# Kernel tuning notes

Hardware: AMD Instinct MI355X
Metric: run time of the kernel (lower is better)

The kernel has to match this reference:

```python
import jax, jax.numpy as jnp
import numpy as np

B, CIN, COUT, H, KS = 16, 64, 64, 224, 7


def setup_inputs() -> dict:
    key = jax.random.key(0)
    k1, k2 = jax.random.split(key)
    x = jax.random.normal(k1, (B, CIN, H, H), dtype=jnp.float32)
    # kaiming_uniform_ default (a=0, fan_in mode): bound = sqrt(6 / fan_in)
    fan_in = CIN * KS * KS
    bound = float(np.sqrt(6.0 / fan_in))
    kernel = jax.random.uniform(k2, (COUT, CIN, KS, KS), minval=-bound, maxval=bound, dtype=jnp.float32)
    return {"input": x, "kernel": kernel}


def _kernel_spectrum(k2d, n):
    # Pad kernel to the optical plane size (n x n), centered, then ifftshift so the
    # frequency-domain product implements a centered circular convolution (4f system).
    ks = k2d.shape[-1]
    s = (n - ks) // 2
    pad = jnp.zeros(k2d.shape[:-2] + (n, n), k2d.dtype)
    pad = pad.at[..., s:s + ks, s:s + ks].set(k2d)
    return jnp.fft.fft2(jnp.fft.ifftshift(pad, axes=(-2, -1)))


def reference(input, kernel):
    n = input.shape[-1]
    # Original loop bug: in_channel index is always 0, so
    # out[b,oc] = optConv2d(sum_ic input[b,ic], kernel[oc,0])
    kf = _kernel_spectrum(kernel[:, 0], n)          # [O, H, W] complex
    sf = jnp.fft.fft2(input.sum(axis=1))            # [B, H, W] complex
    out = jnp.fft.ifft2(sf[:, None] * kf[None]).real  # [B, O, H, W]
    return out.astype(input.dtype)
```

## Files before the change

### kernel.cpp

```cpp
#include <hip/hip_runtime.h>
#include <hip/hip_bf16.h>

#define Hn 224
#define HWn (224*224)
#define B_ 16
#define CIN_ 64
#define COUT_ 64
#define PR 230
#define PC 240
#define PHW (PR*PC)
#define GUARD 1024
#define WOFF (4*1024*1024)

typedef __attribute__((ext_vector_type(4)))  float f32x4;
typedef __attribute__((ext_vector_type(8)))  short bf16x8;
typedef __attribute__((ext_vector_type(16))) float f32x16;

__global__ __launch_bounds__(256) void chan_sum_kernel(const float* __restrict__ x,
                                                       float* __restrict__ Sp) {
    int idx = blockIdx.x * 256 + threadIdx.x;
    const int npix4 = B_ * HWn / 4;
    if (idx >= npix4) return;
    const int s4 = HWn / 4;
    int b  = idx / s4;
    int p4 = idx - b * s4;
    const f32x4* xb = (const f32x4*)x + (size_t)b * CIN_ * s4 + p4;

    f32x4 a0 = __builtin_nontemporal_load(xb + 0 * s4);
    f32x4 a1 = __builtin_nontemporal_load(xb + 1 * s4);
    f32x4 a2 = __builtin_nontemporal_load(xb + 2 * s4);
    f32x4 a3 = __builtin_nontemporal_load(xb + 3 * s4);
    #pragma unroll 4
    for (int c = 4; c < CIN_; c += 4) {
        a0 += __builtin_nontemporal_load(xb + (size_t)(c + 0) * s4);
        a1 += __builtin_nontemporal_load(xb + (size_t)(c + 1) * s4);
        a2 += __builtin_nontemporal_load(xb + (size_t)(c + 2) * s4);
        a3 += __builtin_nontemporal_load(xb + (size_t)(c + 3) * s4);
    }
    f32x4 r = (a0 + a1) + (a2 + a3);

    int y  = p4 / 56;
    int xq = p4 - y * 56;
    float* dst = Sp + (size_t)b * PHW + (size_t)(y + 2) * PC + 2 + xq * 4;
    dst[0] = r.x; dst[1] = r.y; dst[2] = r.z; dst[3] = r.w;
}

__global__ __launch_bounds__(256) void halo_kernel(float* __restrict__ Sp) {
    const int perB = 224 * 6 + 6 * 230;
    int i = blockIdx.x * 256 + threadIdx.x;
    if (i >= perB * B_) return;
    int b = i / perB, t = i - b * perB;
    float* S = Sp + (size_t)b * PHW;
    if (t < 1344) {
        int j = t / 6, c = t - 6 * j;
        int pr = j + 2;
        int p, sp;
        if (c < 2) { p = c;       sp = 224 + c; }
        else       { p = 224 + c; sp = c;       }
        S[pr * PC + p] = S[pr * PC + sp];
    } else {
        t -= 1344;
        int rr = t / 230, p = t - 230 * rr;
        int pr  = (rr < 2) ? rr       : 224 + rr;
        int spr = (rr < 2) ? 224 + rr : rr;
        int sp  = (p < 2) ? p + 224 : (p >= 226 ? p - 224 : p);
        S[pr * PC + p] = S[spr * PC + sp];
    }
}

__global__ __launch_bounds__(256) void wprep_kernel(const float* __restrict__ K,
                                                    unsigned short* __restrict__ W) {
    int i = blockIdx.x * 256 + threadIdx.x;
    if (i >= 64 * 64) return;
    int oc = i >> 6, kk = i & 63;
    int ky = kk >> 3, kx = kk & 7;
    float v = (ky < 7 && kx < 7) ? K[(size_t)oc * (CIN_ * 49) + ky * 7 + kx] : 0.0f;
    __hip_bfloat16 h = __float2bfloat16(v);
    W[i] = *(unsigned short*)&h;
}

__global__ __launch_bounds__(128, 4) void conv_mfma(const float* __restrict__ Sp,
                                                    const unsigned short* __restrict__ W,
                                                    float* __restrict__ out) {
    const int yg = blockIdx.x;
    const int b  = blockIdx.y;
    const int wv = threadIdx.x >> 6;
    const int l  = threadIdx.x & 63;
    const int y   = yg * 2 + wv;
    const int lo5 = l & 31;
    const int hi  = l >> 5;

    bf16x8 afrag[2][4];
    #pragma unroll
    for (int g = 0; g < 2; ++g)
        #pragma unroll
        for (int c = 0; c < 4; ++c)
            afrag[g][c] = *(const bf16x8*)(W + ((g * 32 + lo5) * 64 + c * 16 + hi * 8));

    const float* Sb = Sp + (size_t)b * PHW;
    float* outb = out + (size_t)b * COUT_ * HWn + (size_t)y * Hn;

    for (int xt = 0; xt < 7; ++xt) {
        const int x0 = xt * 32;

        f32x16 acc0, acc1;
        #pragma unroll
        for (int i = 0; i < 16; ++i) { acc0[i] = 0.0f; acc1[i] = 0.0f; }

        #pragma unroll
        for (int c = 0; c < 4; ++c) {
            const int rowg = y + 6 - (2 * c + hi);
            const float* rp = Sb + rowg * PC + x0 + 6 + lo5;
            union { int i[4]; bf16x8 v; } bu;
            #pragma unroll
            for (int j = 0; j < 4; ++j) {
                float flo = rp[-(2 * j)];
                float fhi = rp[-(2 * j) - 1];
                asm("v_cvt_pk_bf16_f32 %0, %1, %2" : "=v"(bu.i[j]) : "v"(flo), "v"(fhi));
            }
            acc0 = __builtin_amdgcn_mfma_f32_32x32x16_bf16(afrag[0][c], bu.v, acc0, 0, 0, 0);
            acc1 = __builtin_amdgcn_mfma_f32_32x32x16_bf16(afrag[1][c], bu.v, acc1, 0, 0, 0);
        }

        #pragma unroll
        for (int r = 0; r < 16; ++r) {
            const int row = (r & 3) + 8 * (r >> 2) + 4 * hi;
            outb[(size_t)row        * HWn + x0 + lo5] = acc0[r];
            outb[(size_t)(32 + row) * HWn + x0 + lo5] = acc1[r];
        }
    }
}

extern "C" void kernel_launch(void* const* d_in, const int* in_sizes, int n_in,
                              void* d_out, int out_size, void* d_ws, size_t ws_size,
                              hipStream_t stream) {
    const float* x = (const float*)d_in[0];
    const float* K = (const float*)d_in[1];
    float* out = (float*)d_out;
    float* Sp = (float*)d_ws + GUARD;
    unsigned short* W = (unsigned short*)((char*)d_ws + WOFF);

    const int npix4 = B_ * HWn / 4;
    chan_sum_kernel<<<(npix4 + 255) / 256, 256, 0, stream>>>(x, Sp);

    const int haloN = B_ * (224 * 6 + 6 * 230);
    halo_kernel<<<(haloN + 255) / 256, 256, 0, stream>>>(Sp);

    wprep_kernel<<<16, 256, 0, stream>>>(K, W);

    dim3 g2(112, 16);
    conv_mfma<<<g2, 128, 0, stream>>>(Sp, W, out);
}
```

Measured before the change: 83.90 us.

## Fuse halo fill into channel sum and weight prep into conv kernel

The circular-wrap halo of the padded sum plane is now written directly by the channel-sum threads that own the edge pixels, which removes the separate halo kernel. The bf16 weight fragments are built inside the conv kernel straight from the fp32 kernel tensor, which removes the weight-prep kernel and its workspace buffer. The intent is to cut two kernel launches and their serialization gaps. In exchange, edge threads in the sum kernel diverge, and every conv block repeats the strided loads and conversion of the weights.

```diff
diff --git a/kernel.cpp b/kernel.cpp
--- a/kernel.cpp
+++ b/kernel.cpp
@@ -10,7 +10,6 @@
 #define PC 240
 #define PHW (PR*PC)
 #define GUARD 1024
-#define WOFF (4*1024*1024)
 
 typedef __attribute__((ext_vector_type(4)))  float f32x4;
 typedef __attribute__((ext_vector_type(8)))  short bf16x8;
@@ -38,49 +37,51 @@
         a3 += __builtin_nontemporal_load(xb + (size_t)(c + 3) * s4);
     }
     f32x4 r = (a0 + a1) + (a2 + a3);
+    float v0 = r.x, v1 = r.y, v2 = r.z, v3 = r.w;
 
     int y  = p4 / 56;
-    int xq = p4 - y * 56;
-    float* dst = Sp + (size_t)b * PHW + (size_t)(y + 2) * PC + 2 + xq * 4;
-    dst[0] = r.x; dst[1] = r.y; dst[2] = r.z; dst[3] = r.w;
-}
+    int x0 = (p4 - y * 56) * 4;
+    float* Sb = Sp + (size_t)b * PHW;
 
-__global__ __launch_bounds__(256) void halo_kernel(float* __restrict__ Sp) {
-    const int perB = 224 * 6 + 6 * 230;
-    int i = blockIdx.x * 256 + threadIdx.x;
-    if (i >= perB * B_) return;
-    int b = i / perB, t = i - b * perB;
-    float* S = Sp + (size_t)b * PHW;
-    if (t < 1344) {
-        int j = t / 6, c = t - 6 * j;
-        int pr = j + 2;
-        int p, sp;
-        if (c < 2) { p = c;       sp = 224 + c; }
-        else       { p = 224 + c; sp = c;       }
-        S[pr * PC + p] = S[pr * PC + sp];
-    } else {
-        t -= 1344;
-        int rr = t / 230, p = t - 230 * rr;
-        int pr  = (rr < 2) ? rr       : 224 + rr;
-        int spr = (rr < 2) ? 224 + rr : rr;
-        int sp  = (p < 2) ? p + 224 : (p >= 226 ? p - 224 : p);
-        S[pr * PC + p] = S[spr * PC + sp];
+    float* dst = Sb + (size_t)(y + 2) * PC + 2 + x0;
+    dst[0] = v0; dst[1] = v1; dst[2] = v2; dst[3] = v3;
+
+    if (y < 4) {
+        float* d = Sb + (size_t)(y + 226) * PC + 2 + x0;
+        d[0] = v0; d[1] = v1; d[2] = v2; d[3] = v3;
+    }
+    if (y >= 222) {
+        float* d = Sb + (size_t)(y - 222) * PC + 2 + x0;
+        d[0] = v0; d[1] = v1; d[2] = v2; d[3] = v3;
+    }
+    if (x0 == 0) {
+        float* d = Sb + (size_t)(y + 2) * PC + 226;
+        d[0] = v0; d[1] = v1; d[2] = v2; d[3] = v3;
+        if (y < 4) {
+            float* e = Sb + (size_t)(y + 226) * PC + 226;
+            e[0] = v0; e[1] = v1; e[2] = v2; e[3] = v3;
+        }
+        if (y >= 222) {
+            float* e = Sb + (size_t)(y - 222) * PC + 226;
+            e[0] = v0; e[1] = v1; e[2] = v2; e[3] = v3;
+        }
+    }
+    if (x0 == 220) {
+        float* d = Sb + (size_t)(y + 2) * PC;
+        d[0] = v2; d[1] = v3;
+        if (y < 4) {
+            float* e = Sb + (size_t)(y + 226) * PC;
+            e[0] = v2; e[1] = v3;
+        }
+        if (y >= 222) {
+            float* e = Sb + (size_t)(y - 222) * PC;
+            e[0] = v2; e[1] = v3;
+        }
     }
 }
 
-__global__ __launch_bounds__(256) void wprep_kernel(const float* __restrict__ K,
-                                                    unsigned short* __restrict__ W) {
-    int i = blockIdx.x * 256 + threadIdx.x;
-    if (i >= 64 * 64) return;
-    int oc = i >> 6, kk = i & 63;
-    int ky = kk >> 3, kx = kk & 7;
-    float v = (ky < 7 && kx < 7) ? K[(size_t)oc * (CIN_ * 49) + ky * 7 + kx] : 0.0f;
-    __hip_bfloat16 h = __float2bfloat16(v);
-    W[i] = *(unsigned short*)&h;
-}
-
 __global__ __launch_bounds__(128, 4) void conv_mfma(const float* __restrict__ Sp,
-                                                    const unsigned short* __restrict__ W,
+                                                    const float* __restrict__ K,
                                                     float* __restrict__ out) {
     const int yg = blockIdx.x;
     const int b  = blockIdx.y;
@@ -92,10 +93,25 @@
 
     bf16x8 afrag[2][4];
     #pragma unroll
-    for (int g = 0; g < 2; ++g)
+    for (int g = 0; g < 2; ++g) {
+        const int m = g * 32 + lo5;
         #pragma unroll
-        for (int c = 0; c < 4; ++c)
-            afrag[g][c] = *(const bf16x8*)(W + ((g * 32 + lo5) * 64 + c * 16 + hi * 8));
+        for (int c = 0; c < 4; ++c) {
+            const int ky = 2 * c + hi;
+            const float* kp = K + (size_t)m * (CIN_ * 49) + ky * 7;
+            const bool ok = (ky < 7);
+            float f0 = ok ? kp[0] : 0.f, f1 = ok ? kp[1] : 0.f;
+            float f2 = ok ? kp[2] : 0.f, f3 = ok ? kp[3] : 0.f;
+            float f4 = ok ? kp[4] : 0.f, f5 = ok ? kp[5] : 0.f;
+            float f6 = ok ? kp[6] : 0.f, f7 = 0.f;
+            union { int i[4]; bf16x8 v; } au;
+            asm("v_cvt_pk_bf16_f32 %0, %1, %2" : "=v"(au.i[0]) : "v"(f0), "v"(f1));
+            asm("v_cvt_pk_bf16_f32 %0, %1, %2" : "=v"(au.i[1]) : "v"(f2), "v"(f3));
+            asm("v_cvt_pk_bf16_f32 %0, %1, %2" : "=v"(au.i[2]) : "v"(f4), "v"(f5));
+            asm("v_cvt_pk_bf16_f32 %0, %1, %2" : "=v"(au.i[3]) : "v"(f6), "v"(f7));
+            afrag[g][c] = au.v;
+        }
+    }
 
     const float* Sb = Sp + (size_t)b * PHW;
     float* outb = out + (size_t)b * COUT_ * HWn + (size_t)y * Hn;
@@ -138,16 +154,10 @@
     const float* K = (const float*)d_in[1];
     float* out = (float*)d_out;
     float* Sp = (float*)d_ws + GUARD;
-    unsigned short* W = (unsigned short*)((char*)d_ws + WOFF);
 
     const int npix4 = B_ * HWn / 4;
     chan_sum_kernel<<<(npix4 + 255) / 256, 256, 0, stream>>>(x, Sp);
 
-    const int haloN = B_ * (224 * 6 + 6 * 230);
-    halo_kernel<<<(haloN + 255) / 256, 256, 0, stream>>>(Sp);
-
-    wprep_kernel<<<16, 256, 0, stream>>>(K, W);
-
     dim3 g2(112, 16);
-    conv_mfma<<<g2, 128, 0, stream>>>(Sp, W, out);
+    conv_mfma<<<g2, 128, 0, stream>>>(Sp, K, out);
 }
```

After: 84.21 us. Within noise of the previous version (+0.4%).

## Fuse halo and weight prep into channel sum; store reversed bf16 planes

Applied to the files above, without the earlier changes.

The channel-sum kernel now converts sums to bf16 and writes them into two column-reversed, parity-offset buffers, handling the circular halo wrap inline. It also absorbs the weight-prep work in extra blocks. This drops two kernel launches. The conv kernel can then load contiguous 32-bit pairs directly as B fragments instead of doing eight strided fp32 loads and conversions. The cost is more scattered 16-bit stores in the sum kernel and a more intricate indexing scheme.

```diff
diff --git a/kernel.cpp b/kernel.cpp
--- a/kernel.cpp
+++ b/kernel.cpp
@@ -6,21 +6,48 @@
 #define B_ 16
 #define CIN_ 64
 #define COUT_ 64
-#define PR 230
-#define PC 240
-#define PHW (PR*PC)
-#define GUARD 1024
-#define WOFF (4*1024*1024)
+#define PCr 240
+#define PRr 230
+#define PHWr (PRr*PCr)
+#define CE 232
+#define CO 233
+#define RE_OFF ((1<<20) + 512)
+#define RO_OFF ((3<<20) + 512)
+#define W_OFF  (6<<20)
 
 typedef __attribute__((ext_vector_type(4)))  float f32x4;
 typedef __attribute__((ext_vector_type(8)))  short bf16x8;
 typedef __attribute__((ext_vector_type(16))) float f32x16;
 
+__device__ __forceinline__ void store_quad(unsigned short* Re, unsigned short* Ro,
+                                           int rowpad, int c0,
+                                           unsigned int q0, unsigned int q1) {
+    unsigned short* pe = Re + rowpad * PCr + (CE - c0 - 3);
+    pe[0] = (unsigned short)q1;
+    pe[1] = (unsigned short)(q1 >> 16);
+    pe[2] = (unsigned short)q0;
+    pe[3] = (unsigned short)(q0 >> 16);
+    unsigned int* po = (unsigned int*)(Ro + rowpad * PCr + (CO - c0 - 3));
+    po[0] = q1;
+    po[1] = q0;
+}
+
 __global__ __launch_bounds__(256) void chan_sum_kernel(const float* __restrict__ x,
-                                                       float* __restrict__ Sp) {
+                                                       unsigned short* __restrict__ Re,
+                                                       unsigned short* __restrict__ Ro,
+                                                       const float* __restrict__ K,
+                                                       unsigned short* __restrict__ W) {
+    if (blockIdx.x >= 784) {
+        int i = (blockIdx.x - 784) * 256 + threadIdx.x;
+        int oc = i >> 6, kk = i & 63;
+        int ky = kk >> 3, kx = kk & 7;
+        float v = (ky < 7 && kx < 7) ? K[(size_t)oc * (CIN_ * 49) + ky * 7 + kx] : 0.0f;
+        __hip_bfloat16 h = __float2bfloat16(v);
+        W[i] = *(unsigned short*)&h;
+        return;
+    }
+
     int idx = blockIdx.x * 256 + threadIdx.x;
-    const int npix4 = B_ * HWn / 4;
-    if (idx >= npix4) return;
     const int s4 = HWn / 4;
     int b  = idx / s4;
     int p4 = idx - b * s4;
@@ -39,47 +66,33 @@
     }
     f32x4 r = (a0 + a1) + (a2 + a3);
 
+    unsigned int q0, q1;
+    asm("v_cvt_pk_bf16_f32 %0, %1, %2" : "=v"(q0) : "v"(r.y), "v"(r.x));
+    asm("v_cvt_pk_bf16_f32 %0, %1, %2" : "=v"(q1) : "v"(r.w), "v"(r.z));
+
     int y  = p4 / 56;
-    int xq = p4 - y * 56;
-    float* dst = Sp + (size_t)b * PHW + (size_t)(y + 2) * PC + 2 + xq * 4;
-    dst[0] = r.x; dst[1] = r.y; dst[2] = r.z; dst[3] = r.w;
-}
+    int c0 = (p4 - y * 56) * 4;
+    unsigned short* Rb_e = Re + (size_t)b * PHWr;
+    unsigned short* Rb_o = Ro + (size_t)b * PHWr;
 
-__global__ __launch_bounds__(256) void halo_kernel(float* __restrict__ Sp) {
-    const int perB = 224 * 6 + 6 * 230;
-    int i = blockIdx.x * 256 + threadIdx.x;
-    if (i >= perB * B_) return;
-    int b = i / perB, t = i - b * perB;
-    float* S = Sp + (size_t)b * PHW;
-    if (t < 1344) {
-        int j = t / 6, c = t - 6 * j;
-        int pr = j + 2;
-        int p, sp;
-        if (c < 2) { p = c;       sp = 224 + c; }
-        else       { p = 224 + c; sp = c;       }
-        S[pr * PC + p] = S[pr * PC + sp];
-    } else {
-        t -= 1344;
-        int rr = t / 230, p = t - 230 * rr;
-        int pr  = (rr < 2) ? rr       : 224 + rr;
-        int spr = (rr < 2) ? 224 + rr : rr;
-        int sp  = (p < 2) ? p + 224 : (p >= 226 ? p - 224 : p);
-        S[pr * PC + p] = S[spr * PC + sp];
+    store_quad(Rb_e, Rb_o, y + 2, c0, q0, q1);
+
+    if (y < 4)   store_quad(Rb_e, Rb_o, y + 226, c0, q0, q1);
+    if (y >= 222) store_quad(Rb_e, Rb_o, y - 222, c0, q0, q1);
+    if (c0 == 0) {
+        store_quad(Rb_e, Rb_o, y + 2, 224, q0, q1);
+        if (y < 4)   store_quad(Rb_e, Rb_o, y + 226, 224, q0, q1);
+        if (y >= 222) store_quad(Rb_e, Rb_o, y - 222, 224, q0, q1);
+    }
+    if (c0 == 220) {
+        store_quad(Rb_e, Rb_o, y + 2, -4, q0, q1);
+        if (y < 4)   store_quad(Rb_e, Rb_o, y + 226, -4, q0, q1);
+        if (y >= 222) store_quad(Rb_e, Rb_o, y - 222, -4, q0, q1);
     }
 }
 
-__global__ __launch_bounds__(256) void wprep_kernel(const float* __restrict__ K,
-                                                    unsigned short* __restrict__ W) {
-    int i = blockIdx.x * 256 + threadIdx.x;
-    if (i >= 64 * 64) return;
-    int oc = i >> 6, kk = i & 63;
-    int ky = kk >> 3, kx = kk & 7;
-    float v = (ky < 7 && kx < 7) ? K[(size_t)oc * (CIN_ * 49) + ky * 7 + kx] : 0.0f;
-    __hip_bfloat16 h = __float2bfloat16(v);
-    W[i] = *(unsigned short*)&h;
-}
-
-__global__ __launch_bounds__(128, 4) void conv_mfma(const float* __restrict__ Sp,
+__global__ __launch_bounds__(128, 4) void conv_mfma(const unsigned short* __restrict__ Re,
+                                                    const unsigned short* __restrict__ Ro,
                                                     const unsigned short* __restrict__ W,
                                                     float* __restrict__ out) {
     const int yg = blockIdx.x;
@@ -97,9 +110,15 @@
         for (int c = 0; c < 4; ++c)
             afrag[g][c] = *(const bf16x8*)(W + ((g * 32 + lo5) * 64 + c * 16 + hi * 8));
 
-    const float* Sb = Sp + (size_t)b * PHW;
+    const unsigned short* revb = ((lo5 & 1) ? Ro : Re) + (size_t)b * PHWr;
+    const int colb = (232 + (lo5 & 1)) - lo5 - 4;
+    int rowoff[4];
+    #pragma unroll
+    for (int c = 0; c < 4; ++c) rowoff[c] = (y + 6 - 2 * c - hi) * PCr;
+
     float* outb = out + (size_t)b * COUT_ * HWn + (size_t)y * Hn;
 
+    #pragma unroll
     for (int xt = 0; xt < 7; ++xt) {
         const int x0 = xt * 32;
 
@@ -109,15 +128,12 @@
 
         #pragma unroll
         for (int c = 0; c < 4; ++c) {
-            const int rowg = y + 6 - (2 * c + hi);
-            const float* rp = Sb + rowg * PC + x0 + 6 + lo5;
-            union { int i[4]; bf16x8 v; } bu;
-            #pragma unroll
-            for (int j = 0; j < 4; ++j) {
-                float flo = rp[-(2 * j)];
-                float fhi = rp[-(2 * j) - 1];
-                asm("v_cvt_pk_bf16_f32 %0, %1, %2" : "=v"(bu.i[j]) : "v"(flo), "v"(fhi));
-            }
+            const unsigned short* p = revb + rowoff[c] + (colb - x0);
+            union { unsigned int i[4]; bf16x8 v; } bu;
+            bu.i[0] = *(const unsigned int*)(p + 0);
+            bu.i[1] = *(const unsigned int*)(p + 2);
+            bu.i[2] = *(const unsigned int*)(p + 4);
+            bu.i[3] = *(const unsigned int*)(p + 6);
             acc0 = __builtin_amdgcn_mfma_f32_32x32x16_bf16(afrag[0][c], bu.v, acc0, 0, 0, 0);
             acc1 = __builtin_amdgcn_mfma_f32_32x32x16_bf16(afrag[1][c], bu.v, acc1, 0, 0, 0);
         }
@@ -137,17 +153,12 @@
     const float* x = (const float*)d_in[0];
     const float* K = (const float*)d_in[1];
     float* out = (float*)d_out;
-    float* Sp = (float*)d_ws + GUARD;
-    unsigned short* W = (unsigned short*)((char*)d_ws + WOFF);
+    unsigned short* Re = (unsigned short*)((char*)d_ws + RE_OFF);
+    unsigned short* Ro = (unsigned short*)((char*)d_ws + RO_OFF);
+    unsigned short* W  = (unsigned short*)((char*)d_ws + W_OFF);
 
-    const int npix4 = B_ * HWn / 4;
-    chan_sum_kernel<<<(npix4 + 255) / 256, 256, 0, stream>>>(x, Sp);
-
-    const int haloN = B_ * (224 * 6 + 6 * 230);
-    halo_kernel<<<(haloN + 255) / 256, 256, 0, stream>>>(Sp);
-
-    wprep_kernel<<<16, 256, 0, stream>>>(K, W);
+    chan_sum_kernel<<<800, 256, 0, stream>>>(x, Re, Ro, K, W);
 
     dim3 g2(112, 16);
-    conv_mfma<<<g2, 128, 0, stream>>>(Sp, W, out);
+    conv_mfma<<<g2, 128, 0, stream>>>(Re, Ro, W, out);
 }
```

Measured after the change: 113.4 us. 1.35x slower.
